# Optimization experiments

Hardware: AMD Instinct MI355X
Metric: run time of the kernel (lower is better)

The kernel has to match this reference:

```python
import jax, jax.numpy as jnp
import numpy as np
from jax import lax

B, C, H, W = 32, 64, 112, 112
ALPHA, BETA1, BETA2 = 0.25, 1.0, 1.0

# STE sign for weights (DifferntiableSign): fwd = +/-1, bwd mask |w|<=1 (w in [-1,1))
@jax.custom_vjp
def dsign(w):
    return jnp.where(w >= 0, 1.0, -1.0).astype(w.dtype)
def _dsign_fwd(w):
    return dsign(w), w
def _dsign_bwd(w, g):
    return (g * ((w < 1) & (w >= -1)).astype(g.dtype),)
dsign.defvjp(_dsign_fwd, _dsign_bwd)

# ReActNet BinaryActivation: fwd = sign(x), bwd piecewise-polynomial STE
@jax.custom_vjp
def bin_act(x):
    return jnp.where(x >= 0, 1.0, -1.0).astype(x.dtype)
def _ba_fwd(x):
    return bin_act(x), x
def _ba_bwd(x, g):
    slope = jnp.where((x >= -1) & (x < 0), 2.0 + 2.0 * x,
             jnp.where((x >= 0) & (x < 1), 2.0 - 2.0 * x, 0.0))
    return (g * slope.astype(g.dtype),)
bin_act.defvjp(_ba_fwd, _ba_bwd)

def scaled_sign_conv(x, w):
    # per-output-channel scale = mean(|w|) over (in, kh, kw)
    scale = jnp.mean(jnp.abs(w), axis=(1, 2, 3), keepdims=True)
    wb = scale * dsign(w)
    return lax.conv_general_dilated(x, wb, window_strides=(1, 1),
                                    padding=((1, 1), (1, 1)),
                                    dimension_numbers=("NCHW", "OIHW", "NCHW"))

def add_bias(x, b):
    return x + b[None, :, None, None]

def prelu(x, a):
    return jnp.where(x >= 0, x, a[None, :, None, None] * x)

def setup_inputs() -> dict:
    key = jax.random.key(0)
    ks = jax.random.split(key, 12)
    x = jax.random.normal(ks[0], (B, C, H, W), dtype=jnp.float32)
    # conv weights: symmetric uniform in [-1e-3, 1e-3] so signs are nontrivial
    w3 = (jax.random.uniform(ks[1], (C, C, 3, 3)) - 0.5) * 0.002
    w_pw = (jax.random.uniform(ks[2], (C, C, 3, 3)) - 0.5) * 0.002
    b11 = jax.random.normal(ks[3], (C,)) * 0.01
    b12 = jax.random.normal(ks[4], (C,)) * 0.01
    b13 = jax.random.normal(ks[5], (C,)) * 0.01
    b21 = jax.random.normal(ks[6], (C,)) * 0.01
    b22 = jax.random.normal(ks[7], (C,)) * 0.01
    b23 = jax.random.normal(ks[8], (C,)) * 0.01
    a1 = jax.random.uniform(ks[9], (C,), minval=0.1, maxval=0.4)
    a2 = jax.random.uniform(ks[10], (C,), minval=0.1, maxval=0.4)
    return {"x": x, "w3": w3, "w_pw": w_pw, "b11": b11, "b12": b12, "b13": b13,
            "b21": b21, "b22": b22, "b23": b23, "a1": a1, "a2": a2}

def reference(x, w3, w_pw, b11, b12, b13, b21, b22, b23, a1, a2):
    x_in = x * BETA1
    out1 = add_bias(x_in, b11)            # move11
    out1 = bin_act(out1)
    out1 = scaled_sign_conv(out1, w3)     # binary_3x3
    out1 = x + out1 * ALPHA               # stride==1: residual is original x
    out1 = add_bias(out1, b12)            # move12
    out1 = prelu(out1, a1)
    out1 = add_bias(out1, b13)            # move13
    out1_in = out1 * BETA2
    out2 = add_bias(out1_in, b21)         # move21
    out2 = bin_act(out2)
    out2 = scaled_sign_conv(out2, w_pw)   # binary_pw (3x3 per given defaults)
    out2 = out2 * ALPHA + out1
    out2 = add_bias(out2, b22)            # move22
    out2 = prelu(out2, a2)
    out2 = add_bias(out2, b23)            # move23
    return out2
```

## Files before the change

kernel.cpp:

```cpp
#include <hip/hip_runtime.h>
#include <hip/hip_fp16.h>
#include <stdint.h>

#define Bn 32
#define Cc 64
#define Hh 112
#define Ww 112
#define HWp (Hh*Ww)
#define NPIX (Bn*HWp)
#define PW 114
#define PHW (PW*PW)
#define NPAIR (HWp/2)
#define WROW (Ww/2)
#define ALPHA 0.25f

typedef float    f32x2 __attribute__((ext_vector_type(2)));
typedef _Float16 f16x2 __attribute__((ext_vector_type(2)));

#define WB1_OFF   0
#define WB2_OFF   4608
#define ASC1_OFF  9216
#define ASC2_OFF  9472
#define CI1_OFF   9728
#define CI2_OFF   12288
#define BITS1_OFF 16384
#define BITS2_OFF (16384 + 3326976)
#define OUT1H_OFF (16384 + 2*3326976)
#define WS_NEED   (OUT1H_OFF + (size_t)NPIX*Cc*2)

#define MEMFENCE() asm volatile("" ::: "memory")

__global__ __launch_bounds__(64) void prep_weights(
        const float* __restrict__ w3, const float* __restrict__ wpw,
        uint64_t* __restrict__ wb1, uint64_t* __restrict__ wb2,
        float* __restrict__ asc1, float* __restrict__ asc2,
        int* __restrict__ ci1, int* __restrict__ ci2) {
    int b = blockIdx.x;
    int lane = threadIdx.x;
    const float* w  = (b < 64) ? w3   : wpw;
    uint64_t* wbits = (b < 64) ? wb1  : wb2;
    float*    ascp  = (b < 64) ? asc1 : asc2;
    int*      cip   = (b < 64) ? ci1  : ci2;
    int o = b & 63;
    const float* wp = w + ((size_t)o * Cc + lane) * 9;
    float v[9]; float asum = 0.f;
    #pragma unroll
    for (int t = 0; t < 9; ++t) { v[t] = wp[t]; asum += fabsf(v[t]); }
    uint64_t bal[9];
    #pragma unroll
    for (int t = 0; t < 9; ++t) bal[t] = __ballot(v[t] < 0.f);
    if (lane < 9) {
        wbits[o * 9 + lane] = bal[lane];
        int ty = lane, tr = ty / 3, tc = ty % 3;
        int sum = 0;
        #pragma unroll
        for (int t = 0; t < 9; ++t) {
            int r = t / 3, c = t % 3;
            bool inv = (tr == 0 && r == 0) || (tr == 2 && r == 2) ||
                       (tc == 0 && c == 0) || (tc == 2 && c == 2);
            if (inv) sum += 64 - 2 * (int)__popcll(bal[t]);
        }
        cip[o * 10 + ty] = 576 - sum;
    }
    #pragma unroll
    for (int off = 32; off > 0; off >>= 1) asum += __shfl_down(asum, off, 64);
    if (lane == 0) ascp[o] = ALPHA * asum * (1.f / 576.f);
}

__global__ __launch_bounds__(256, 4) void pack1(const float* __restrict__ x,
                                                const float* __restrict__ b11,
                                                uint64_t* __restrict__ bits1,
                                                uint64_t* __restrict__ bits2) {
    int n = blockIdx.y;
    if (blockIdx.x >= 25) {
        int t = (blockIdx.x - 25) * 256 + threadIdx.x;
        if (t < 2 * PW + 2 * Hh) {
            int cell;
            if      (t < PW)          cell = t;
            else if (t < 2 * PW)      cell = 113 * PW + (t - PW);
            else if (t < 2 * PW + Hh) cell = (t - 2 * PW + 1) * PW;
            else                      cell = (t - 2 * PW - Hh + 1) * PW + 113;
            size_t bi = (size_t)n * PHW + cell;
            bits1[bi] = 0; bits2[bi] = 0;
        }
        return;
    }
    int p = blockIdx.x * 256 + threadIdx.x;
    if (p >= NPAIR) return;
    int h = p / WROW, w0 = (p - h * WROW) * 2;
    int hw = h * Ww + w0;
    const float* xp = x + (size_t)n * Cc * HWp + hw;
    size_t bi = (size_t)n * PHW + (h + 1) * PW + (w0 + 1);

    f32x2 cur[16], nxt[16];
    #pragma unroll
    for (int j = 0; j < 16; ++j) cur[j] = *(const f32x2*)(xp + (size_t)j * HWp);

    uint64_t ma = 0, mb = 0;
    #pragma unroll 1
    for (int cc = 0; cc < Cc - 16; cc += 16) {
        #pragma unroll
        for (int j = 0; j < 16; ++j)
            nxt[j] = *(const f32x2*)(xp + (size_t)(cc + 16 + j) * HWp);
        MEMFENCE();
        #pragma unroll
        for (int j = 0; j < 16; ++j) {
            float bb = b11[cc + j];
            if (cur[j].x + bb < 0.f) ma |= (1ull << (cc + j));
            if (cur[j].y + bb < 0.f) mb |= (1ull << (cc + j));
        }
        MEMFENCE();
        #pragma unroll
        for (int j = 0; j < 16; ++j) cur[j] = nxt[j];
    }
    #pragma unroll
    for (int j = 0; j < 16; ++j) {
        float bb = b11[48 + j];
        if (cur[j].x + bb < 0.f) ma |= (1ull << (48 + j));
        if (cur[j].y + bb < 0.f) mb |= (1ull << (48 + j));
    }
    bits1[bi] = ma; bits1[bi + 1] = mb;
}

template <typename OutT>
__global__ __launch_bounds__(256, 4) void conv1_ep(
        const float* __restrict__ x, const uint64_t* __restrict__ bits1,
        const uint64_t* __restrict__ wb, const float* __restrict__ asc,
        const int* __restrict__ cint,
        const float* __restrict__ b12, const float* __restrict__ a1,
        const float* __restrict__ b13, const float* __restrict__ b21,
        OutT* __restrict__ out1, uint64_t* __restrict__ bits2) {
    __shared__ int lci[Cc * 10];
    for (int i = threadIdx.x; i < Cc * 10; i += 256) lci[i] = cint[i];
    __syncthreads();

    int p = blockIdx.x * 256 + threadIdx.x;
    if (p >= NPAIR) return;
    int n = blockIdx.y;
    int h = p / WROW, w0 = (p - h * WROW) * 2;
    int hw = h * Ww + w0;
    int rowp = (h == 0) ? 0 : (h == Hh - 1) ? 6 : 3;
    int t9a = rowp + ((w0 == 0) ? 0 : 1);
    int t9b = rowp + ((w0 + 1 == Ww - 1) ? 2 : 1);

    const uint64_t* bp = bits1 + (size_t)n * PHW + (h + 1) * PW + (w0 + 1);
    uint64_t q0[4], q1[4], q2[4];
    #pragma unroll
    for (int c = 0; c < 4; ++c) {
        q0[c] = bp[-PW - 1 + c]; q1[c] = bp[-1 + c]; q2[c] = bp[PW - 1 + c];
    }

    const float* xp = x + (size_t)n * Cc * HWp + hw;
    OutT* op = out1 + (size_t)n * Cc * HWp + hw;
    uint64_t m2a = 0, m2b = 0;

    f32x2 cur[8], nxt[8];
    #pragma unroll
    for (int j = 0; j < 8; ++j) cur[j] = *(const f32x2*)(xp + (size_t)j * HWp);

    #pragma unroll 1
    for (int oc = 0; oc <= Cc - 8; oc += 8) {
        if (oc < Cc - 8) {
            #pragma unroll
            for (int j = 0; j < 8; ++j)
                nxt[j] = *(const f32x2*)(xp + (size_t)(oc + 8 + j) * HWp);
        }
        MEMFENCE();
        #pragma unroll
        for (int j = 0; j < 8; ++j) {
            int o = oc + j;
            const uint64_t* wo = wb + o * 9;
            uint64_t t0 = wo[0], t1 = wo[1], t2 = wo[2], t3 = wo[3], t4 = wo[4],
                     t5 = wo[5], t6 = wo[6], t7 = wo[7], t8 = wo[8];
            int sa = (int)__popcll(q0[0] ^ t0) + (int)__popcll(q0[1] ^ t1) + (int)__popcll(q0[2] ^ t2)
                   + (int)__popcll(q1[0] ^ t3) + (int)__popcll(q1[1] ^ t4) + (int)__popcll(q1[2] ^ t5)
                   + (int)__popcll(q2[0] ^ t6) + (int)__popcll(q2[1] ^ t7) + (int)__popcll(q2[2] ^ t8);
            int sb = (int)__popcll(q0[1] ^ t0) + (int)__popcll(q0[2] ^ t1) + (int)__popcll(q0[3] ^ t2)
                   + (int)__popcll(q1[1] ^ t3) + (int)__popcll(q1[2] ^ t4) + (int)__popcll(q1[3] ^ t5)
                   + (int)__popcll(q2[1] ^ t6) + (int)__popcll(q2[2] ^ t7) + (int)__popcll(q2[3] ^ t8);
            int ca = lci[o * 10 + t9a];
            int cb = lci[o * 10 + t9b];
            float sc = asc[o], B2 = b12[o], A = a1[o], B3 = b13[o], B1 = b21[o];
            float va = fmaf(sc, (float)(ca - 2 * sa), cur[j].x);
            float vb = fmaf(sc, (float)(cb - 2 * sb), cur[j].y);
            va += B2; va = va >= 0.f ? va : A * va; va += B3;
            vb += B2; vb = vb >= 0.f ? vb : A * vb; vb += B3;
            if constexpr (sizeof(OutT) == 2) {
                f16x2 hv; hv.x = (_Float16)va; hv.y = (_Float16)vb;
                *(f16x2*)(op + (size_t)o * HWp) = hv;
            } else {
                f32x2 fv; fv.x = va; fv.y = vb;
                *(f32x2*)(op + (size_t)o * HWp) = fv;
            }
            if (va + B1 < 0.f) m2a |= (1ull << o);
            if (vb + B1 < 0.f) m2b |= (1ull << o);
        }
        MEMFENCE();
        #pragma unroll
        for (int j = 0; j < 8; ++j) cur[j] = nxt[j];
    }
    size_t b2 = (size_t)n * PHW + (h + 1) * PW + (w0 + 1);
    bits2[b2] = m2a; bits2[b2 + 1] = m2b;
}

template <typename InT>
__global__ __launch_bounds__(256, 4) void conv2_ep(
        const uint64_t* __restrict__ bits2, const InT* __restrict__ out1,
        const uint64_t* __restrict__ wb, const float* __restrict__ asc,
        const int* __restrict__ cint,
        const float* __restrict__ b22, const float* __restrict__ a2,
        const float* __restrict__ b23, float* __restrict__ out) {
    __shared__ int lci[Cc * 10];
    for (int i = threadIdx.x; i < Cc * 10; i += 256) lci[i] = cint[i];
    __syncthreads();

    int p = blockIdx.x * 256 + threadIdx.x;
    if (p >= NPAIR) return;
    int n = blockIdx.y;
    int h = p / WROW, w0 = (p - h * WROW) * 2;
    int hw = h * Ww + w0;
    int rowp = (h == 0) ? 0 : (h == Hh - 1) ? 6 : 3;
    int t9a = rowp + ((w0 == 0) ? 0 : 1);
    int t9b = rowp + ((w0 + 1 == Ww - 1) ? 2 : 1);

    const uint64_t* bp = bits2 + (size_t)n * PHW + (h + 1) * PW + (w0 + 1);
    uint64_t q0[4], q1[4], q2[4];
    #pragma unroll
    for (int c = 0; c < 4; ++c) {
        q0[c] = bp[-PW - 1 + c]; q1[c] = bp[-1 + c]; q2[c] = bp[PW - 1 + c];
    }

    const InT* ip = out1 + (size_t)n * Cc * HWp + hw;
    float* op = out + (size_t)n * Cc * HWp + hw;

    f16x2 curh[8], nxth[8];
    f32x2 curf[8], nxtf[8];
    if constexpr (sizeof(InT) == 2) {
        #pragma unroll
        for (int j = 0; j < 8; ++j) curh[j] = *(const f16x2*)(ip + (size_t)j * HWp);
    } else {
        #pragma unroll
        for (int j = 0; j < 8; ++j) curf[j] = *(const f32x2*)(ip + (size_t)j * HWp);
    }

    #pragma unroll 1
    for (int oc = 0; oc <= Cc - 8; oc += 8) {
        if (oc < Cc - 8) {
            if constexpr (sizeof(InT) == 2) {
                #pragma unroll
                for (int j = 0; j < 8; ++j)
                    nxth[j] = *(const f16x2*)(ip + (size_t)(oc + 8 + j) * HWp);
            } else {
                #pragma unroll
                for (int j = 0; j < 8; ++j)
                    nxtf[j] = *(const f32x2*)(ip + (size_t)(oc + 8 + j) * HWp);
            }
        }
        MEMFENCE();
        #pragma unroll
        for (int j = 0; j < 8; ++j) {
            int o = oc + j;
            const uint64_t* wo = wb + o * 9;
            uint64_t t0 = wo[0], t1 = wo[1], t2 = wo[2], t3 = wo[3], t4 = wo[4],
                     t5 = wo[5], t6 = wo[6], t7 = wo[7], t8 = wo[8];
            int sa = (int)__popcll(q0[0] ^ t0) + (int)__popcll(q0[1] ^ t1) + (int)__popcll(q0[2] ^ t2)
                   + (int)__popcll(q1[0] ^ t3) + (int)__popcll(q1[1] ^ t4) + (int)__popcll(q1[2] ^ t5)
                   + (int)__popcll(q2[0] ^ t6) + (int)__popcll(q2[1] ^ t7) + (int)__popcll(q2[2] ^ t8);
            int sb = (int)__popcll(q0[1] ^ t0) + (int)__popcll(q0[2] ^ t1) + (int)__popcll(q0[3] ^ t2)
                   + (int)__popcll(q1[1] ^ t3) + (int)__popcll(q1[2] ^ t4) + (int)__popcll(q1[3] ^ t5)
                   + (int)__popcll(q2[1] ^ t6) + (int)__popcll(q2[2] ^ t7) + (int)__popcll(q2[3] ^ t8);
            int ca = lci[o * 10 + t9a];
            int cb = lci[o * 10 + t9b];
            float ra, rb;
            if constexpr (sizeof(InT) == 2) { ra = (float)curh[j].x; rb = (float)curh[j].y; }
            else                            { ra = curf[j].x;        rb = curf[j].y; }
            float sc = asc[o], B2 = b22[o], A = a2[o], B3 = b23[o];
            float va = fmaf(sc, (float)(ca - 2 * sa), ra);
            float vb = fmaf(sc, (float)(cb - 2 * sb), rb);
            va += B2; va = va >= 0.f ? va : A * va; va += B3;
            vb += B2; vb = vb >= 0.f ? vb : A * vb; vb += B3;
            f32x2 fv; fv.x = va; fv.y = vb;
            __builtin_nontemporal_store(fv, (f32x2*)(op + (size_t)o * HWp));
        }
        MEMFENCE();
        if constexpr (sizeof(InT) == 2) {
            #pragma unroll
            for (int j = 0; j < 8; ++j) curh[j] = nxth[j];
        } else {
            #pragma unroll
            for (int j = 0; j < 8; ++j) curf[j] = nxtf[j];
        }
    }
}

extern "C" void kernel_launch(void* const* d_in, const int* in_sizes, int n_in,
                              void* d_out, int out_size, void* d_ws, size_t ws_size,
                              hipStream_t stream) {
    const float* x    = (const float*)d_in[0];
    const float* w3   = (const float*)d_in[1];
    const float* wpw  = (const float*)d_in[2];
    const float* b11  = (const float*)d_in[3];
    const float* b12  = (const float*)d_in[4];
    const float* b13  = (const float*)d_in[5];
    const float* b21  = (const float*)d_in[6];
    const float* b22  = (const float*)d_in[7];
    const float* b23  = (const float*)d_in[8];
    const float* a1   = (const float*)d_in[9];
    const float* a2   = (const float*)d_in[10];

    char* ws = (char*)d_ws;
    uint64_t* wb1   = (uint64_t*)(ws + WB1_OFF);
    uint64_t* wb2   = (uint64_t*)(ws + WB2_OFF);
    float*    asc1  = (float*)(ws + ASC1_OFF);
    float*    asc2  = (float*)(ws + ASC2_OFF);
    int*      ci1   = (int*)(ws + CI1_OFF);
    int*      ci2   = (int*)(ws + CI2_OFF);
    uint64_t* bits1 = (uint64_t*)(ws + BITS1_OFF);
    uint64_t* bits2 = (uint64_t*)(ws + BITS2_OFF);
    float*    out   = (float*)d_out;

    dim3 pgrid(27, Bn);
    dim3 cgrid((NPAIR + 255) / 256, Bn);

    prep_weights<<<128, 64, 0, stream>>>(w3, wpw, wb1, wb2, asc1, asc2, ci1, ci2);
    pack1<<<pgrid, 256, 0, stream>>>(x, b11, bits1, bits2);

    if (ws_size >= WS_NEED) {
        __half* out1h = (__half*)(ws + OUT1H_OFF);
        conv1_ep<__half><<<cgrid, 256, 0, stream>>>(x, bits1, wb1, asc1, ci1,
                                                    b12, a1, b13, b21, out1h, bits2);
        conv2_ep<__half><<<cgrid, 256, 0, stream>>>(bits2, out1h, wb2, asc2, ci2,
                                                    b22, a2, b23, out);
    } else {
        conv1_ep<float><<<cgrid, 256, 0, stream>>>(x, bits1, wb1, asc1, ci1,
                                                   b12, a1, b13, b21, out, bits2);
        conv2_ep<float><<<cgrid, 256, 0, stream>>>(bits2, out, wb2, asc2, ci2,
                                                   b22, a2, b23, out);
    }
}
```

Baseline: 294.7 us.

## Split output channels across grid z-dimension in pack and conv kernels

Adds a z grid dimension so pack1 processes 32 channels per block and each conv kernel handles 16 output channels per block, writing partial bitmasks as 32-bit or 16-bit sub-words. This raises the number of blocks fourfold and removes the serial channel loop with its software-pipelined prefetch, aiming at more memory-level parallelism and better occupancy. Each block still loads the 3x3 neighbourhood bit words, so those reads are repeated per channel group. PReLU is rewritten as an fma with fminf to avoid a select.

```diff
diff --git a/kernel.cpp b/kernel.cpp
--- a/kernel.cpp
+++ b/kernel.cpp
@@ -13,6 +13,8 @@
 #define NPAIR (HWp/2)
 #define WROW (Ww/2)
 #define ALPHA 0.25f
+#define CSP 4
+#define CPB (Cc/CSP)
 
 typedef float    f32x2 __attribute__((ext_vector_type(2)));
 typedef _Float16 f16x2 __attribute__((ext_vector_type(2)));
@@ -72,7 +74,9 @@
                                                 uint64_t* __restrict__ bits1,
                                                 uint64_t* __restrict__ bits2) {
     int n = blockIdx.y;
+    int z = blockIdx.z;
     if (blockIdx.x >= 25) {
+        if (z) return;
         int t = (blockIdx.x - 25) * 256 + threadIdx.x;
         if (t < 2 * PW + 2 * Hh) {
             int cell;
@@ -89,37 +93,25 @@
     if (p >= NPAIR) return;
     int h = p / WROW, w0 = (p - h * WROW) * 2;
     int hw = h * Ww + w0;
-    const float* xp = x + (size_t)n * Cc * HWp + hw;
+    int cb = z * 32;
+    const float* xp = x + ((size_t)n * Cc + cb) * HWp + hw;
     size_t bi = (size_t)n * PHW + (h + 1) * PW + (w0 + 1);
 
-    f32x2 cur[16], nxt[16];
-    #pragma unroll
-    for (int j = 0; j < 16; ++j) cur[j] = *(const f32x2*)(xp + (size_t)j * HWp);
-
-    uint64_t ma = 0, mb = 0;
-    #pragma unroll 1
-    for (int cc = 0; cc < Cc - 16; cc += 16) {
-        #pragma unroll
-        for (int j = 0; j < 16; ++j)
-            nxt[j] = *(const f32x2*)(xp + (size_t)(cc + 16 + j) * HWp);
-        MEMFENCE();
-        #pragma unroll
-        for (int j = 0; j < 16; ++j) {
-            float bb = b11[cc + j];
-            if (cur[j].x + bb < 0.f) ma |= (1ull << (cc + j));
-            if (cur[j].y + bb < 0.f) mb |= (1ull << (cc + j));
-        }
-        MEMFENCE();
-        #pragma unroll
-        for (int j = 0; j < 16; ++j) cur[j] = nxt[j];
-    }
-    #pragma unroll
-    for (int j = 0; j < 16; ++j) {
-        float bb = b11[48 + j];
-        if (cur[j].x + bb < 0.f) ma |= (1ull << (48 + j));
-        if (cur[j].y + bb < 0.f) mb |= (1ull << (48 + j));
-    }
-    bits1[bi] = ma; bits1[bi + 1] = mb;
+    f32x2 v[32];
+    #pragma unroll
+    for (int j = 0; j < 32; ++j) v[j] = *(const f32x2*)(xp + (size_t)j * HWp);
+    MEMFENCE();
+
+    uint32_t ma = 0, mb = 0;
+    #pragma unroll
+    for (int j = 0; j < 32; ++j) {
+        float bb = b11[cb + j];
+        if (v[j].x + bb < 0.f) ma |= (1u << j);
+        if (v[j].y + bb < 0.f) mb |= (1u << j);
+    }
+    uint32_t* wp1 = (uint32_t*)(bits1 + bi);
+    wp1[z]     = ma;
+    wp1[2 + z] = mb;
 }
 
 template <typename OutT>
@@ -130,8 +122,10 @@
         const float* __restrict__ b12, const float* __restrict__ a1,
         const float* __restrict__ b13, const float* __restrict__ b21,
         OutT* __restrict__ out1, uint64_t* __restrict__ bits2) {
-    __shared__ int lci[Cc * 10];
-    for (int i = threadIdx.x; i < Cc * 10; i += 256) lci[i] = cint[i];
+    __shared__ int lci[CPB * 10];
+    int zb = blockIdx.z;
+    int ob = zb * CPB;
+    for (int i = threadIdx.x; i < CPB * 10; i += 256) lci[i] = cint[ob * 10 + i];
     __syncthreads();
 
     int p = blockIdx.x * 256 + threadIdx.x;
@@ -150,57 +144,47 @@
         q0[c] = bp[-PW - 1 + c]; q1[c] = bp[-1 + c]; q2[c] = bp[PW - 1 + c];
     }
 
-    const float* xp = x + (size_t)n * Cc * HWp + hw;
-    OutT* op = out1 + (size_t)n * Cc * HWp + hw;
-    uint64_t m2a = 0, m2b = 0;
-
-    f32x2 cur[8], nxt[8];
-    #pragma unroll
-    for (int j = 0; j < 8; ++j) cur[j] = *(const f32x2*)(xp + (size_t)j * HWp);
-
-    #pragma unroll 1
-    for (int oc = 0; oc <= Cc - 8; oc += 8) {
-        if (oc < Cc - 8) {
-            #pragma unroll
-            for (int j = 0; j < 8; ++j)
-                nxt[j] = *(const f32x2*)(xp + (size_t)(oc + 8 + j) * HWp);
+    const float* xp = x + ((size_t)n * Cc + ob) * HWp + hw;
+    OutT* op = out1 + ((size_t)n * Cc + ob) * HWp + hw;
+
+    f32x2 cur[CPB];
+    #pragma unroll
+    for (int j = 0; j < CPB; ++j) cur[j] = *(const f32x2*)(xp + (size_t)j * HWp);
+    MEMFENCE();
+
+    uint32_t m2a = 0, m2b = 0;
+    #pragma unroll
+    for (int j = 0; j < CPB; ++j) {
+        int o = ob + j;
+        const uint64_t* wo = wb + o * 9;
+        uint64_t t0 = wo[0], t1 = wo[1], t2 = wo[2], t3 = wo[3], t4 = wo[4],
+                 t5 = wo[5], t6 = wo[6], t7 = wo[7], t8 = wo[8];
+        int sa = (int)__popcll(q0[0] ^ t0) + (int)__popcll(q0[1] ^ t1) + (int)__popcll(q0[2] ^ t2)
+               + (int)__popcll(q1[0] ^ t3) + (int)__popcll(q1[1] ^ t4) + (int)__popcll(q1[2] ^ t5)
+               + (int)__popcll(q2[0] ^ t6) + (int)__popcll(q2[1] ^ t7) + (int)__popcll(q2[2] ^ t8);
+        int sb = (int)__popcll(q0[1] ^ t0) + (int)__popcll(q0[2] ^ t1) + (int)__popcll(q0[3] ^ t2)
+               + (int)__popcll(q1[1] ^ t3) + (int)__popcll(q1[2] ^ t4) + (int)__popcll(q1[3] ^ t5)
+               + (int)__popcll(q2[1] ^ t6) + (int)__popcll(q2[2] ^ t7) + (int)__popcll(q2[3] ^ t8);
+        int ca = lci[j * 10 + t9a];
+        int cb = lci[j * 10 + t9b];
+        float sc = asc[o], B2 = b12[o], Am1 = a1[o] - 1.0f, B3 = b13[o], B1 = b21[o];
+        float va = fmaf(sc, (float)(ca - 2 * sa), cur[j].x);
+        float vb = fmaf(sc, (float)(cb - 2 * sb), cur[j].y);
+        va += B2; va = fmaf(fminf(va, 0.f), Am1, va); va += B3;
+        vb += B2; vb = fmaf(fminf(vb, 0.f), Am1, vb); vb += B3;
+        if constexpr (sizeof(OutT) == 2) {
+            f16x2 hv; hv.x = (_Float16)va; hv.y = (_Float16)vb;
+            *(f16x2*)(op + (size_t)j * HWp) = hv;
+        } else {
+            f32x2 fv; fv.x = va; fv.y = vb;
+            *(f32x2*)(op + (size_t)j * HWp) = fv;
         }
-        MEMFENCE();
-        #pragma unroll
-        for (int j = 0; j < 8; ++j) {
-            int o = oc + j;
-            const uint64_t* wo = wb + o * 9;
-            uint64_t t0 = wo[0], t1 = wo[1], t2 = wo[2], t3 = wo[3], t4 = wo[4],
-                     t5 = wo[5], t6 = wo[6], t7 = wo[7], t8 = wo[8];
-            int sa = (int)__popcll(q0[0] ^ t0) + (int)__popcll(q0[1] ^ t1) + (int)__popcll(q0[2] ^ t2)
-                   + (int)__popcll(q1[0] ^ t3) + (int)__popcll(q1[1] ^ t4) + (int)__popcll(q1[2] ^ t5)
-                   + (int)__popcll(q2[0] ^ t6) + (int)__popcll(q2[1] ^ t7) + (int)__popcll(q2[2] ^ t8);
-            int sb = (int)__popcll(q0[1] ^ t0) + (int)__popcll(q0[2] ^ t1) + (int)__popcll(q0[3] ^ t2)
-                   + (int)__popcll(q1[1] ^ t3) + (int)__popcll(q1[2] ^ t4) + (int)__popcll(q1[3] ^ t5)
-                   + (int)__popcll(q2[1] ^ t6) + (int)__popcll(q2[2] ^ t7) + (int)__popcll(q2[3] ^ t8);
-            int ca = lci[o * 10 + t9a];
-            int cb = lci[o * 10 + t9b];
-            float sc = asc[o], B2 = b12[o], A = a1[o], B3 = b13[o], B1 = b21[o];
-            float va = fmaf(sc, (float)(ca - 2 * sa), cur[j].x);
-            float vb = fmaf(sc, (float)(cb - 2 * sb), cur[j].y);
-            va += B2; va = va >= 0.f ? va : A * va; va += B3;
-            vb += B2; vb = vb >= 0.f ? vb : A * vb; vb += B3;
-            if constexpr (sizeof(OutT) == 2) {
-                f16x2 hv; hv.x = (_Float16)va; hv.y = (_Float16)vb;
-                *(f16x2*)(op + (size_t)o * HWp) = hv;
-            } else {
-                f32x2 fv; fv.x = va; fv.y = vb;
-                *(f32x2*)(op + (size_t)o * HWp) = fv;
-            }
-            if (va + B1 < 0.f) m2a |= (1ull << o);
-            if (vb + B1 < 0.f) m2b |= (1ull << o);
-        }
-        MEMFENCE();
-        #pragma unroll
-        for (int j = 0; j < 8; ++j) cur[j] = nxt[j];
-    }
-    size_t b2 = (size_t)n * PHW + (h + 1) * PW + (w0 + 1);
-    bits2[b2] = m2a; bits2[b2 + 1] = m2b;
+        if (va + B1 < 0.f) m2a |= (1u << j);
+        if (vb + B1 < 0.f) m2b |= (1u << j);
+    }
+    uint16_t* b2p = (uint16_t*)(bits2 + (size_t)n * PHW + (h + 1) * PW + (w0 + 1));
+    b2p[zb]     = (uint16_t)m2a;
+    b2p[4 + zb] = (uint16_t)m2b;
 }
 
 template <typename InT>
@@ -210,8 +194,10 @@
         const int* __restrict__ cint,
         const float* __restrict__ b22, const float* __restrict__ a2,
         const float* __restrict__ b23, float* __restrict__ out) {
-    __shared__ int lci[Cc * 10];
-    for (int i = threadIdx.x; i < Cc * 10; i += 256) lci[i] = cint[i];
+    __shared__ int lci[CPB * 10];
+    int zb = blockIdx.z;
+    int ob = zb * CPB;
+    for (int i = threadIdx.x; i < CPB * 10; i += 256) lci[i] = cint[ob * 10 + i];
     __syncthreads();
 
     int p = blockIdx.x * 256 + threadIdx.x;
@@ -230,66 +216,44 @@
         q0[c] = bp[-PW - 1 + c]; q1[c] = bp[-1 + c]; q2[c] = bp[PW - 1 + c];
     }
 
-    const InT* ip = out1 + (size_t)n * Cc * HWp + hw;
-    float* op = out + (size_t)n * Cc * HWp + hw;
-
-    f16x2 curh[8], nxth[8];
-    f32x2 curf[8], nxtf[8];
+    const InT* ip = out1 + ((size_t)n * Cc + ob) * HWp + hw;
+    float* op = out + ((size_t)n * Cc + ob) * HWp + hw;
+
+    f16x2 curh[CPB];
+    f32x2 curf[CPB];
     if constexpr (sizeof(InT) == 2) {
         #pragma unroll
-        for (int j = 0; j < 8; ++j) curh[j] = *(const f16x2*)(ip + (size_t)j * HWp);
+        for (int j = 0; j < CPB; ++j) curh[j] = *(const f16x2*)(ip + (size_t)j * HWp);
     } else {
         #pragma unroll
-        for (int j = 0; j < 8; ++j) curf[j] = *(const f32x2*)(ip + (size_t)j * HWp);
-    }
-
-    #pragma unroll 1
-    for (int oc = 0; oc <= Cc - 8; oc += 8) {
-        if (oc < Cc - 8) {
-            if constexpr (sizeof(InT) == 2) {
-                #pragma unroll
-                for (int j = 0; j < 8; ++j)
-                    nxth[j] = *(const f16x2*)(ip + (size_t)(oc + 8 + j) * HWp);
-            } else {
-                #pragma unroll
-                for (int j = 0; j < 8; ++j)
-                    nxtf[j] = *(const f32x2*)(ip + (size_t)(oc + 8 + j) * HWp);
-            }
-        }
-        MEMFENCE();
-        #pragma unroll
-        for (int j = 0; j < 8; ++j) {
-            int o = oc + j;
-            const uint64_t* wo = wb + o * 9;
-            uint64_t t0 = wo[0], t1 = wo[1], t2 = wo[2], t3 = wo[3], t4 = wo[4],
-                     t5 = wo[5], t6 = wo[6], t7 = wo[7], t8 = wo[8];
-            int sa = (int)__popcll(q0[0] ^ t0) + (int)__popcll(q0[1] ^ t1) + (int)__popcll(q0[2] ^ t2)
-                   + (int)__popcll(q1[0] ^ t3) + (int)__popcll(q1[1] ^ t4) + (int)__popcll(q1[2] ^ t5)
-                   + (int)__popcll(q2[0] ^ t6) + (int)__popcll(q2[1] ^ t7) + (int)__popcll(q2[2] ^ t8);
-            int sb = (int)__popcll(q0[1] ^ t0) + (int)__popcll(q0[2] ^ t1) + (int)__popcll(q0[3] ^ t2)
-                   + (int)__popcll(q1[1] ^ t3) + (int)__popcll(q1[2] ^ t4) + (int)__popcll(q1[3] ^ t5)
-                   + (int)__popcll(q2[1] ^ t6) + (int)__popcll(q2[2] ^ t7) + (int)__popcll(q2[3] ^ t8);
-            int ca = lci[o * 10 + t9a];
-            int cb = lci[o * 10 + t9b];
-            float ra, rb;
-            if constexpr (sizeof(InT) == 2) { ra = (float)curh[j].x; rb = (float)curh[j].y; }
-            else                            { ra = curf[j].x;        rb = curf[j].y; }
-            float sc = asc[o], B2 = b22[o], A = a2[o], B3 = b23[o];
-            float va = fmaf(sc, (float)(ca - 2 * sa), ra);
-            float vb = fmaf(sc, (float)(cb - 2 * sb), rb);
-            va += B2; va = va >= 0.f ? va : A * va; va += B3;
-            vb += B2; vb = vb >= 0.f ? vb : A * vb; vb += B3;
-            f32x2 fv; fv.x = va; fv.y = vb;
-            __builtin_nontemporal_store(fv, (f32x2*)(op + (size_t)o * HWp));
-        }
-        MEMFENCE();
-        if constexpr (sizeof(InT) == 2) {
-            #pragma unroll
-            for (int j = 0; j < 8; ++j) curh[j] = nxth[j];
-        } else {
-            #pragma unroll
-            for (int j = 0; j < 8; ++j) curf[j] = nxtf[j];
-        }
+        for (int j = 0; j < CPB; ++j) curf[j] = *(const f32x2*)(ip + (size_t)j * HWp);
+    }
+    MEMFENCE();
+
+    #pragma unroll
+    for (int j = 0; j < CPB; ++j) {
+        int o = ob + j;
+        const uint64_t* wo = wb + o * 9;
+        uint64_t t0 = wo[0], t1 = wo[1], t2 = wo[2], t3 = wo[3], t4 = wo[4],
+                 t5 = wo[5], t6 = wo[6], t7 = wo[7], t8 = wo[8];
+        int sa = (int)__popcll(q0[0] ^ t0) + (int)__popcll(q0[1] ^ t1) + (int)__popcll(q0[2] ^ t2)
+               + (int)__popcll(q1[0] ^ t3) + (int)__popcll(q1[1] ^ t4) + (int)__popcll(q1[2] ^ t5)
+               + (int)__popcll(q2[0] ^ t6) + (int)__popcll(q2[1] ^ t7) + (int)__popcll(q2[2] ^ t8);
+        int sb = (int)__popcll(q0[1] ^ t0) + (int)__popcll(q0[2] ^ t1) + (int)__popcll(q0[3] ^ t2)
+               + (int)__popcll(q1[1] ^ t3) + (int)__popcll(q1[2] ^ t4) + (int)__popcll(q1[3] ^ t5)
+               + (int)__popcll(q2[1] ^ t6) + (int)__popcll(q2[2] ^ t7) + (int)__popcll(q2[3] ^ t8);
+        int ca = lci[j * 10 + t9a];
+        int cb = lci[j * 10 + t9b];
+        float ra, rb;
+        if constexpr (sizeof(InT) == 2) { ra = (float)curh[j].x; rb = (float)curh[j].y; }
+        else                            { ra = curf[j].x;        rb = curf[j].y; }
+        float sc = asc[o], B2 = b22[o], Am1 = a2[o] - 1.0f, B3 = b23[o];
+        float va = fmaf(sc, (float)(ca - 2 * sa), ra);
+        float vb = fmaf(sc, (float)(cb - 2 * sb), rb);
+        va += B2; va = fmaf(fminf(va, 0.f), Am1, va); va += B3;
+        vb += B2; vb = fmaf(fminf(vb, 0.f), Am1, vb); vb += B3;
+        f32x2 fv; fv.x = va; fv.y = vb;
+        __builtin_nontemporal_store(fv, (f32x2*)(op + (size_t)j * HWp));
     }
 }
 
@@ -319,8 +283,8 @@
     uint64_t* bits2 = (uint64_t*)(ws + BITS2_OFF);
     float*    out   = (float*)d_out;
 
-    dim3 pgrid(27, Bn);
-    dim3 cgrid((NPAIR + 255) / 256, Bn);
+    dim3 pgrid(27, Bn, 2);
+    dim3 cgrid((NPAIR + 255) / 256, Bn, CSP);
 
     prep_weights<<<128, 64, 0, stream>>>(w3, wpw, wb1, wb2, asc1, asc2, ci1, ci2);
     pack1<<<pgrid, 256, 0, stream>>>(x, b11, bits1, bits2);
```

Result: faster. 272.2 us (-7.6%).
